# Optimization experiments

Hardware: AMD Instinct MI355X
Metric: run time of the kernel (lower is better)

The kernel has to match this reference:

```python
import jax, jax.numpy as jnp
import numpy as np

N_HIDDEN = 8
N_CLASSES = 10
TIME_STEPS = 28
INPUT_DIM = 28
FORGET_BIAS = 1.0


def setup_inputs() -> dict:
    key = jax.random.key(0)
    k1, k2, k3, k4 = jax.random.split(key, 4)
    B = 32768
    x = jax.random.normal(k1, (B, TIME_STEPS, INPUT_DIM), dtype=jnp.float32)
    # BasicLSTMCell kernel: [input_dim + hidden, 4*hidden], gate order i, j, f, o
    W_lstm = jax.random.normal(k2, (INPUT_DIM + N_HIDDEN, 4 * N_HIDDEN), dtype=jnp.float32) * 0.1
    b_lstm = jnp.zeros((4 * N_HIDDEN,), dtype=jnp.float32)  # TF zero-init bias
    out_weights = jax.random.normal(k3, (N_HIDDEN, N_CLASSES), dtype=jnp.float32)
    out_biases = jax.random.normal(k4, (N_CLASSES,), dtype=jnp.float32)
    return {"x": x, "W_lstm": W_lstm, "b_lstm": b_lstm,
            "out_weights": out_weights, "out_biases": out_biases}


def reference(x, W_lstm, b_lstm, out_weights, out_biases):
    B = x.shape[0]

    def step(carry, xt):
        c, h = carry
        gates = jnp.concatenate([xt, h], axis=-1) @ W_lstm + b_lstm  # [B, 4H]
        i, j, f, o = jnp.split(gates, 4, axis=-1)  # BasicLSTMCell order: i, j, f, o
        new_c = c * jax.nn.sigmoid(f + FORGET_BIAS) + jax.nn.sigmoid(i) * jnp.tanh(j)
        new_h = jnp.tanh(new_c) * jax.nn.sigmoid(o)
        return (new_c, new_h), None

    xs = jnp.swapaxes(x, 0, 1)  # [T, B, input_dim]
    init = (jnp.zeros((B, N_HIDDEN), x.dtype), jnp.zeros((B, N_HIDDEN), x.dtype))
    (_, last_h), _ = jax.lax.scan(step, init, xs)
    logits = last_h @ out_weights + out_biases  # [B, n_classes]
    return logits
```

## Files before the change

kernel.cpp:

```cpp
#include <hip/hip_runtime.h>


#define TSTEPS 28
#define DIN    28
#define NH     8
#define NG     32
#define NC     10
#define NROWS  36
#define EPB    8
#define XQ_PER_ELEM (TSTEPS * 7)

__device__ __forceinline__ float fexp2(float x) { return __builtin_amdgcn_exp2f(x); }
__device__ __forceinline__ float frcp(float x)  { return __builtin_amdgcn_rcpf(x); }

#define SWZ(v, imm) \
    __int_as_float(__builtin_amdgcn_ds_swizzle(__float_as_int(v), (imm)))

__global__ __launch_bounds__(256, 4) void lstm_kernel(
    const float* __restrict__ x,
    const float* __restrict__ W,
    const float* __restrict__ bias,
    const float* __restrict__ Wout,
    const float* __restrict__ bout,
    float* __restrict__ out)
{
    __shared__ float4 xs[EPB * XQ_PER_ELEM];

    const int g   = threadIdx.x >> 5;
    const int l5  = threadIdx.x & 31;
    const int gt  = l5 >> 3;
    const int e   = blockIdx.x * EPB + g;

    {
        const float4* gx = (const float4*)(x + (size_t)blockIdx.x *
                                           (EPB * TSTEPS * DIN));
#pragma unroll
        for (int i = 0; i < 7; ++i) {
            int idx = threadIdx.x + i * 256;
            if (idx < EPB * XQ_PER_ELEM) xs[idx] = gx[idx];
        }
    }

    float Wr[NROWS];
#pragma unroll
    for (int k = 0; k < NROWS; ++k) Wr[k] = W[k * NG + l5];
#pragma unroll
    for (int k = 0; k < NROWS; ++k) asm volatile("" : "+v"(Wr[k]));

    const float bg = bias[l5] + (gt == 2 ? 1.0f : 0.0f);
    const float sK = (gt == 1) ?  2.8853900817779268f : -1.4426950408889634f;
    const float mK = (gt == 1) ? -2.0f : 1.0f;
    const float qK = (gt == 1) ?  1.0f : 0.0f;

    float c = 0.0f;
    float hall[NH];
#pragma unroll
    for (int j = 0; j < NH; ++j) hall[j] = 0.0f;

    __syncthreads();

    const float4* xrow = xs + g * XQ_PER_ELEM;

#pragma unroll 2
    for (int t = 0; t < TSTEPS; ++t) {
        float4 xq[7];
#pragma unroll
        for (int i = 0; i < 7; ++i) xq[i] = xrow[t * 7 + i];

        float g0 = bg, g1 = 0.0f, g2 = 0.0f, g3 = 0.0f;
#pragma unroll
        for (int i = 0; i < 7; ++i) {
            g0 = fmaf(xq[i].x, Wr[4*i+0], g0);
            g1 = fmaf(xq[i].y, Wr[4*i+1], g1);
            g2 = fmaf(xq[i].z, Wr[4*i+2], g2);
            g3 = fmaf(xq[i].w, Wr[4*i+3], g3);
        }
#pragma unroll
        for (int k = 0; k < NH; k += 4) {
            g0 = fmaf(hall[k+0], Wr[DIN+k+0], g0);
            g1 = fmaf(hall[k+1], Wr[DIN+k+1], g1);
            g2 = fmaf(hall[k+2], Wr[DIN+k+2], g2);
            g3 = fmaf(hall[k+3], Wr[DIN+k+3], g3);
        }
        float gsum = (g0 + g1) + (g2 + g3);

        float a = fmaf(mK, frcp(1.0f + fexp2(sK * gsum)), qK);

        float iv = SWZ(a, 0x0007);
        float jv = SWZ(a, 0x0107);
        float fv = SWZ(a, 0x0207);
        float ov = SWZ(a, 0x0307);

        c = fmaf(c, fv, iv * jv);
        float th = fmaf(-2.0f,
                        frcp(1.0f + fexp2(2.8853900817779268f * c)),
                        1.0f);
        float hu = th * ov;

        hall[0] = SWZ(hu, 0x0000);
        hall[1] = SWZ(hu, 0x0020);
        hall[2] = SWZ(hu, 0x0040);
        hall[3] = SWZ(hu, 0x0060);
        hall[4] = SWZ(hu, 0x0080);
        hall[5] = SWZ(hu, 0x00A0);
        hall[6] = SWZ(hu, 0x00C0);
        hall[7] = SWZ(hu, 0x00E0);
    }

    if (l5 < NC) {
        float acc = bout[l5];
#pragma unroll
        for (int k = 0; k < NH; ++k)
            acc = fmaf(hall[k], Wout[k * NC + l5], acc);
        out[(size_t)e * NC + l5] = acc;
    }
}

extern "C" void kernel_launch(void* const* d_in, const int* in_sizes, int n_in,
                              void* d_out, int out_size, void* d_ws, size_t ws_size,
                              hipStream_t stream) {
    const float* x    = (const float*)d_in[0];
    const float* W    = (const float*)d_in[1];
    const float* b    = (const float*)d_in[2];
    const float* Wout = (const float*)d_in[3];
    const float* bout = (const float*)d_in[4];
    float* out = (float*)d_out;

    const int B = in_sizes[0] / (TSTEPS * DIN);
    const int grid = B / EPB;
    lstm_kernel<<<grid, 256, 0, stream>>>(x, W, b, Wout, bout, out);
}
```

Baseline: 185.4 us.

## Replace per-step h broadcast swizzles with DPP row-rotate chain

Each thread now keeps only its own hidden value and rotates it across the 8-lane group with DPP row_ror:1, using a per-lane permuted copy of the recurrent weights so every rotated value meets the matching weight. This replaces eight ds_swizzle broadcasts per timestep, which go through the LDS crossbar, with cheaper DPP moves, and cuts live registers from the hall array. Launch bounds rise to 6 waves per SIMD to use the freed registers. The rotation chain is serial, which adds dependency latency within each step.

Result: no change. 182.7 us (-1.5%).

```diff
diff --git a/kernel.cpp b/kernel.cpp
--- a/kernel.cpp
+++ b/kernel.cpp
@@ -6,7 +6,6 @@
 #define NH     8
 #define NG     32
 #define NC     10
-#define NROWS  36
 #define EPB    8
 #define XQ_PER_ELEM (TSTEPS * 7)
 
@@ -16,7 +15,13 @@
 #define SWZ(v, imm) \
     __int_as_float(__builtin_amdgcn_ds_swizzle(__float_as_int(v), (imm)))
 
-__global__ __launch_bounds__(256, 4) void lstm_kernel(
+__device__ __forceinline__ float dpp_ror1(float v) {
+    int i = __float_as_int(v);
+    return __int_as_float(
+        __builtin_amdgcn_update_dpp(i, i, 0x121, 0xF, 0xF, true));
+}
+
+__global__ __launch_bounds__(256, 6) void lstm_kernel(
     const float* __restrict__ x,
     const float* __restrict__ W,
     const float* __restrict__ bias,
@@ -28,6 +33,7 @@
 
     const int g   = threadIdx.x >> 5;
     const int l5  = threadIdx.x & 31;
+    const int u   = l5 & 7;
     const int gt  = l5 >> 3;
     const int e   = blockIdx.x * EPB + g;
 
@@ -41,11 +47,17 @@
         }
     }
 
-    float Wr[NROWS];
+    float Wx[DIN];
 #pragma unroll
-    for (int k = 0; k < NROWS; ++k) Wr[k] = W[k * NG + l5];
+    for (int k = 0; k < DIN; ++k) Wx[k] = W[k * NG + l5];
+    float Wh[NH];
 #pragma unroll
-    for (int k = 0; k < NROWS; ++k) asm volatile("" : "+v"(Wr[k]));
+    for (int s = 0; s < NH; ++s)
+        Wh[s] = W[(DIN + ((u - s + 8) & 7)) * NG + l5];
+#pragma unroll
+    for (int k = 0; k < DIN; ++k) asm volatile("" : "+v"(Wx[k]));
+#pragma unroll
+    for (int s = 0; s < NH; ++s) asm volatile("" : "+v"(Wh[s]));
 
     const float bg = bias[l5] + (gt == 2 ? 1.0f : 0.0f);
     const float sK = (gt == 1) ?  2.8853900817779268f : -1.4426950408889634f;
@@ -53,9 +65,7 @@
     const float qK = (gt == 1) ?  1.0f : 0.0f;
 
     float c = 0.0f;
-    float hall[NH];
-#pragma unroll
-    for (int j = 0; j < NH; ++j) hall[j] = 0.0f;
+    float hprev = 0.0f;
 
     __syncthreads();
 
@@ -70,17 +80,22 @@
         float g0 = bg, g1 = 0.0f, g2 = 0.0f, g3 = 0.0f;
 #pragma unroll
         for (int i = 0; i < 7; ++i) {
-            g0 = fmaf(xq[i].x, Wr[4*i+0], g0);
-            g1 = fmaf(xq[i].y, Wr[4*i+1], g1);
-            g2 = fmaf(xq[i].z, Wr[4*i+2], g2);
-            g3 = fmaf(xq[i].w, Wr[4*i+3], g3);
+            g0 = fmaf(xq[i].x, Wx[4*i+0], g0);
+            g1 = fmaf(xq[i].y, Wx[4*i+1], g1);
+            g2 = fmaf(xq[i].z, Wx[4*i+2], g2);
+            g3 = fmaf(xq[i].w, Wx[4*i+3], g3);
         }
-#pragma unroll
-        for (int k = 0; k < NH; k += 4) {
-            g0 = fmaf(hall[k+0], Wr[DIN+k+0], g0);
-            g1 = fmaf(hall[k+1], Wr[DIN+k+1], g1);
-            g2 = fmaf(hall[k+2], Wr[DIN+k+2], g2);
-            g3 = fmaf(hall[k+3], Wr[DIN+k+3], g3);
+
+        {
+            float hc = hprev;
+            g0 = fmaf(hc, Wh[0], g0);
+            hc = dpp_ror1(hc); g1 = fmaf(hc, Wh[1], g1);
+            hc = dpp_ror1(hc); g2 = fmaf(hc, Wh[2], g2);
+            hc = dpp_ror1(hc); g3 = fmaf(hc, Wh[3], g3);
+            hc = dpp_ror1(hc); g0 = fmaf(hc, Wh[4], g0);
+            hc = dpp_ror1(hc); g1 = fmaf(hc, Wh[5], g1);
+            hc = dpp_ror1(hc); g2 = fmaf(hc, Wh[6], g2);
+            hc = dpp_ror1(hc); g3 = fmaf(hc, Wh[7], g3);
         }
         float gsum = (g0 + g1) + (g2 + g3);
 
@@ -95,17 +110,18 @@
         float th = fmaf(-2.0f,
                         frcp(1.0f + fexp2(2.8853900817779268f * c)),
                         1.0f);
-        float hu = th * ov;
+        hprev = th * ov;
+    }
 
-        hall[0] = SWZ(hu, 0x0000);
-        hall[1] = SWZ(hu, 0x0020);
-        hall[2] = SWZ(hu, 0x0040);
-        hall[3] = SWZ(hu, 0x0060);
-        hall[4] = SWZ(hu, 0x0080);
-        hall[5] = SWZ(hu, 0x00A0);
-        hall[6] = SWZ(hu, 0x00C0);
-        hall[7] = SWZ(hu, 0x00E0);
-    }
+    float hall[NH];
+    hall[0] = SWZ(hprev, 0x0000);
+    hall[1] = SWZ(hprev, 0x0020);
+    hall[2] = SWZ(hprev, 0x0040);
+    hall[3] = SWZ(hprev, 0x0060);
+    hall[4] = SWZ(hprev, 0x0080);
+    hall[5] = SWZ(hprev, 0x00A0);
+    hall[6] = SWZ(hprev, 0x00C0);
+    hall[7] = SWZ(hprev, 0x00E0);
 
     if (l5 < NC) {
         float acc = bout[l5];
```
